# Performance work log

Hardware: AMD Instinct MI355X
Metric: run time of the kernel (lower is better)

## Reference

```python
import jax, jax.numpy as jnp
import numpy as np

COST_CLASS, COST_BBOX, COST_GIOU = 2.0, 5.0, 2.0
ALPHA, GAMMA = 0.25, 2.0
EPS = 1e-8
N_CANDIDATE = 10


def box_cxcywh_to_xyxy(b):
    cx, cy, w, h = b[..., 0], b[..., 1], b[..., 2], b[..., 3]
    return jnp.stack([cx - 0.5 * w, cy - 0.5 * h, cx + 0.5 * w, cy + 0.5 * h], axis=-1)


def pairwise_iou_giou(b1, b2):
    # b1: [N,4] xyxy, b2: [M,4] xyxy -> iou [N,M], giou [N,M]
    area1 = (b1[:, 2] - b1[:, 0]) * (b1[:, 3] - b1[:, 1])
    area2 = (b2[:, 2] - b2[:, 0]) * (b2[:, 3] - b2[:, 1])
    lt = jnp.maximum(b1[:, None, :2], b2[None, :, :2])
    rb = jnp.minimum(b1[:, None, 2:], b2[None, :, 2:])
    wh = jnp.clip(rb - lt, 0.0)
    inter = wh[..., 0] * wh[..., 1]
    union = area1[:, None] + area2[None, :] - inter
    iou = inter / (union + EPS)
    # smallest enclosing box
    lt_c = jnp.minimum(b1[:, None, :2], b2[None, :, :2])
    rb_c = jnp.maximum(b1[:, None, 2:], b2[None, :, 2:])
    wh_c = jnp.clip(rb_c - lt_c, 0.0)
    area_c = wh_c[..., 0] * wh_c[..., 1]
    giou = iou - (area_c - union) / (area_c + EPS)
    return iou, giou


def _match_one(logits, boxes, labels, tboxes):
    # logits [Q,C], boxes [Q,4] cxcywh, labels [G] int, tboxes [G,4] cxcywh
    Q = logits.shape[0]
    G = labels.shape[0]
    prob = jax.nn.sigmoid(logits)                 # [Q,C]  (use_focal_loss path)
    p = prob[:, labels]                           # [Q,G] gather at GT classes
    neg_cost = (1.0 - ALPHA) * p ** GAMMA * (-jnp.log1p(-p + EPS))
    pos_cost = ALPHA * (1.0 - p) ** GAMMA * (-jnp.log(p + EPS))
    cost_class = pos_cost - neg_cost              # [Q,G]
    cost_bbox = jnp.sum(jnp.abs(boxes[:, None, :] - tboxes[None, :, :]), axis=-1)  # L1 cdist [Q,G]
    iou, giou = pairwise_iou_giou(box_cxcywh_to_xyxy(boxes), box_cxcywh_to_xyxy(tboxes))
    C = COST_BBOX * cost_bbox + COST_CLASS * cost_class + COST_GIOU * (-giou)      # [Q,G]

    # --- SimOTA matching (simota_matching), vectorized over GT ---
    cost = C.T                                    # [G,Q]
    ious = iou.T                                  # [G,Q]
    n_cand = min(N_CANDIDATE, Q)
    topk_ious, _ = jax.lax.top_k(ious, n_cand)    # [G,n_cand]
    dynamic_ks = jnp.clip(jnp.sum(topk_ious, axis=1).astype(jnp.int32), 1)  # [G]
    # rank of each anchor per GT under ascending cost
    ranks = jnp.argsort(jnp.argsort(cost, axis=1), axis=1)                  # [G,Q]
    matching = (ranks < dynamic_ks[:, None]).astype(cost.dtype)             # [G,Q]
    # resolve anchors matched to multiple GTs: keep argmin-cost GT
    anchor_matching_gt = matching.sum(axis=0)     # [Q]
    cost_argmin = jnp.argmin(cost, axis=0)        # [Q]
    onehot_min = (jnp.arange(G)[:, None] == cost_argmin[None, :]).astype(cost.dtype)
    matching = jnp.where(anchor_matching_gt[None, :] > 1, onehot_min, matching)
    return jnp.stack([cost, matching], axis=0)    # [2,G,Q]


def reference(pred_logits, pred_boxes, tgt_labels, tgt_boxes):
    # per-image cost blocks + SimOTA matching matrices: [bs, 2, G, Q]
    return jax.vmap(_match_one)(pred_logits, pred_boxes, tgt_labels, tgt_boxes)


def setup_inputs() -> dict:
    key = jax.random.key(0)
    k1, k2, k3, k4 = jax.random.split(key, 4)
    bs, Q, C, G = 16, 4000, 80, 128
    pred_logits = jax.random.normal(k1, (bs, Q, C), dtype=jnp.float32)
    pred_boxes = jax.random.uniform(k2, (bs, Q, 4), dtype=jnp.float32, minval=0.05, maxval=0.95)
    tgt_labels = jax.random.randint(k3, (bs, G), 0, C)
    tgt_boxes = jax.random.uniform(k4, (bs, G, 4), dtype=jnp.float32, minval=0.05, maxval=0.95)
    return {"pred_logits": pred_logits, "pred_boxes": pred_boxes,
            "tgt_labels": tgt_labels, "tgt_boxes": tgt_boxes}
```

## Files before the change

### kernel.cpp

```cpp
#include <hip/hip_runtime.h>
#include <cmath>
#include <cfloat>
#include <climits>


static constexpr int BS = 16;
static constexpr int Qn = 4000;
static constexpr int Cn = 80;
static constexpr int Gn = 128;
static constexpr float kEPS = 1e-8f;


static constexpr size_t kThrvOff = 0;
static constexpr size_t kThriOff = 8 * 1024;
static constexpr size_t kFOff    = 16 * 1024;
static constexpr size_t kFBytes  = (size_t)BS * Cn * Qn * sizeof(float);

__device__ __forceinline__ float focal_cost(float l) {
    const float p = 1.0f / (1.0f + expf(-l));
    const float neg = (0.75f * (p * p)) * (-log1pf(-p + kEPS));
    const float pos = (0.25f * ((1.0f - p) * (1.0f - p))) * (-logf(p + kEPS));
    return pos - neg;
}

__global__ __launch_bounds__(256) void kP_focal(
    const float* __restrict__ logits,
    float* __restrict__ F)
{
    const int b  = blockIdx.y;
    const int q0 = blockIdx.x * 32;
    const int t  = threadIdx.x;

    __shared__ float s_f[32 * 81];

    const float* src = logits + ((size_t)b * Qn + q0) * Cn;
#pragma unroll
    for (int i = 0; i < 10; ++i) {
        const int idx = t + i * 256;
        const int ql = idx / 80, c = idx % 80;
        s_f[ql * 81 + c] = focal_cost(src[idx]);
    }
    __syncthreads();

    float* dst = F + (size_t)b * Cn * Qn;
#pragma unroll
    for (int i = 0; i < 10; ++i) {
        const int j = t + i * 256;
        const int c = j >> 5, ql = j & 31;
        dst[(size_t)c * Qn + q0 + ql] = s_f[ql * 81 + c];
    }
}

__device__ __forceinline__ unsigned long long pack_ci(float c, int q) {
    const unsigned int u = __float_as_uint(c + 0.0f);
    const unsigned int s = (u & 0x80000000u) ? ~u : (u | 0x80000000u);
    return ((unsigned long long)s << 32) | (unsigned int)q;
}

__device__ __forceinline__ unsigned long long shfl_xor_u64(unsigned long long v, int m) {
    const int lo = __shfl_xor((int)(unsigned int)v, m, 64);
    const int hi = __shfl_xor((int)(unsigned int)(v >> 32), m, 64);
    return ((unsigned long long)(unsigned int)hi << 32) | (unsigned int)lo;
}

__device__ __forceinline__ unsigned long long bitonic64_asc_u64(unsigned long long v, int lane) {
#pragma unroll
    for (int k = 2; k <= 64; k <<= 1) {
#pragma unroll
        for (int j = 32; j >= 1; j >>= 1) {
            if (j < k) {
                const unsigned long long o = shfl_xor_u64(v, j);
                const bool up = ((lane & k) == 0);
                const bool keepmin = (((lane & j) == 0) == up);
                const bool omin = (o < v);
                v = (keepmin == omin) ? o : v;
            }
        }
    }
    return v;
}

__device__ __forceinline__ float bitonic64_asc_f32(float v, int lane) {
#pragma unroll
    for (int k = 2; k <= 64; k <<= 1) {
#pragma unroll
        for (int j = 32; j >= 1; j >>= 1) {
            if (j < k) {
                const float o = __shfl_xor(v, j, 64);
                const bool up = ((lane & k) == 0);
                const bool keepmin = (((lane & j) == 0) == up);
                const bool omin = (o < v);
                v = (keepmin == omin) ? o : v;
            }
        }
    }
    return v;
}

__device__ __forceinline__ void ins10_vi(float (&cv)[10], int (&ci)[10],
                                         float v, int q) {
    bool le[10];
#pragma unroll
    for (int j = 0; j < 10; ++j) le[j] = (cv[j] <= v);
#pragma unroll
    for (int j = 9; j >= 1; --j) {
        const float nv = le[j] ? cv[j] : (le[j - 1] ? v : cv[j - 1]);
        const int   ni = le[j] ? ci[j] : (le[j - 1] ? q : ci[j - 1]);
        cv[j] = nv; ci[j] = ni;
    }
    if (!le[0]) { cv[0] = v; ci[0] = q; }
}

__device__ __forceinline__ void ins10_desc(float (&iv)[10], float v) {
    bool ge[10];
#pragma unroll
    for (int j = 0; j < 10; ++j) ge[j] = (iv[j] >= v);
#pragma unroll
    for (int j = 9; j >= 1; --j)
        iv[j] = ge[j] ? iv[j] : (ge[j - 1] ? v : iv[j - 1]);
    if (!ge[0]) iv[0] = v;
}

template <bool USE_F>
__global__ __launch_bounds__(512, 8) void kF(
    const float* __restrict__ boxes,
    const int*   __restrict__ labels,
    const float* __restrict__ tboxes,
    const float* __restrict__ logits,
    const float* __restrict__ F,
    float* __restrict__ out,
    float* __restrict__ thrv,
    int*   __restrict__ thri)
{
    const int lane = threadIdx.x & 63;
    const int w8   = threadIdx.x >> 6;
    const int sub  = w8 & 3;
    const int r    = blockIdx.x;
    const int b    = r >> 7;
    const int g    = r & (Gn - 1);

    const float* tb = tboxes + (size_t)r * 4;
    const float tcx = tb[0], tcy = tb[1], tw = tb[2], th = tb[3];
    const float tx0 = tcx - 0.5f * tw, ty0 = tcy - 0.5f * th;
    const float tx1 = tcx + 0.5f * tw, ty1 = tcy + 0.5f * th;
    const float tarea = (tx1 - tx0) * (ty1 - ty0);

    const float4* brow = reinterpret_cast<const float4*>(boxes) + (size_t)b * Qn;

    __shared__ float              s_st[8][1024];
    __shared__ unsigned long long s_ccb[4][64];
    __shared__ float              s_icb[4][64];
    __shared__ int                s_cnt[8];
    __shared__ unsigned long long s_ce[4][12];
    __shared__ float              s_if[4][12];

    if (lane == 0) s_cnt[w8] = 0;

    if (w8 < 4) {
        const int lab = labels[r];
        const float* Frow = USE_F ? (F + ((size_t)b * Cn + lab) * Qn) : nullptr;
        const float* lcol = USE_F ? nullptr : (logits + (size_t)b * Qn * Cn + lab);
        float* crow = out + (size_t)(b * 2) * Gn * Qn + (size_t)g * Qn;

        float m0 = INFINITY, m1 = INFINITY;

#pragma unroll
        for (int it = 0; it < 4; ++it) {
            const int q0 = it * 1024 + sub * 256 + (lane << 2);
            if ((it < 3) || (q0 < Qn)) {
                float cls4[4];
                if (USE_F) {
                    const float4 f4 = *reinterpret_cast<const float4*>(Frow + q0);
                    cls4[0] = f4.x; cls4[1] = f4.y; cls4[2] = f4.z; cls4[3] = f4.w;
                } else {
#pragma unroll
                    for (int e = 0; e < 4; ++e)
                        cls4[e] = focal_cost(lcol[(size_t)(q0 + e) * Cn]);
                }
                float c4[4];
#pragma unroll
                for (int e = 0; e < 4; ++e) {
                    const float cls = cls4[e];
                    const float4 bb = brow[q0 + e];
                    const float cx = bb.x, cy = bb.y, w = bb.z, h = bb.w;
                    const float x0 = cx - 0.5f * w, y0 = cy - 0.5f * h;
                    const float x1 = cx + 0.5f * w, y1 = cy + 0.5f * h;
                    const float area1 = (x1 - x0) * (y1 - y0);
                    const float l1 = ((fabsf(cx - tcx) + fabsf(cy - tcy))
                                      + fabsf(w - tw)) + fabsf(h - th);
                    const float ltx = fmaxf(x0, tx0), lty = fmaxf(y0, ty0);
                    const float rbx = fminf(x1, tx1), rby = fminf(y1, ty1);
                    const float iw = fmaxf(rbx - ltx, 0.0f), ih = fmaxf(rby - lty, 0.0f);
                    const float inter = iw * ih;
                    const float uni = (area1 + tarea) - inter;
                    const float iou = inter / (uni + kEPS);
                    const float cltx = fminf(x0, tx0), clty = fminf(y0, ty0);
                    const float crbx = fmaxf(x1, tx1), crby = fmaxf(y1, ty1);
                    const float cw = fmaxf(crbx - cltx, 0.0f), ch = fmaxf(crby - clty, 0.0f);
                    const float areac = cw * ch;
                    const float giou = iou - (areac - uni) / (areac + kEPS);

                    const float cost = (5.0f * l1 + 2.0f * cls) + 2.0f * (-giou);
                    c4[e] = cost;
                    const bool le0 = (m0 <= cost), le1 = (m1 <= cost);
                    m1 = le1 ? m1 : (le0 ? cost : m0);
                    m0 = le0 ? m0 : cost;
                }
                float4 cv4; cv4.x = c4[0]; cv4.y = c4[1]; cv4.z = c4[2]; cv4.w = c4[3];
                *reinterpret_cast<float4*>(crow + q0) = cv4;
                *reinterpret_cast<float4*>(&s_st[w8][it * 256 + (lane << 2)]) = cv4;
            }
        }

        float T = 0.0f;
#pragma unroll
        for (int t = 0; t < 10; ++t) {
            float m = m0;
#pragma unroll
            for (int d = 1; d <= 32; d <<= 1)
                m = fminf(m, __shfl_xor(m, d, 64));
            T = m;
            const bool own0 = (m0 == m);
            const unsigned long long bal = __ballot(own0);
            if (own0 && lane == __ffsll((long long)bal) - 1) { m0 = m1; m1 = INFINITY; }
        }

#pragma unroll
        for (int it = 0; it < 4; ++it) {
            const int q0 = it * 1024 + sub * 256 + (lane << 2);
            if ((it < 3) || (q0 < Qn)) {
                const float4 c4 = *reinterpret_cast<const float4*>(
                    &s_st[w8][it * 256 + (lane << 2)]);
#pragma unroll
                for (int e = 0; e < 4; ++e) {
                    const float c = (e == 0) ? c4.x : (e == 1) ? c4.y
                                  : (e == 2) ? c4.z : c4.w;
                    if (c <= T) {
                        const int slot = atomicAdd(&s_cnt[w8], 1);
                        if (slot < 64) s_ccb[sub][slot] = pack_ci(c, q0 + e);
                    }
                }
            }
        }

        const int cnt = s_cnt[w8];
        if (cnt <= 64) {
            unsigned long long v = (lane < cnt) ? s_ccb[sub][lane] : ~0ull;
            v = bitonic64_asc_u64(v, lane);
            if (lane < 12) s_ce[sub][lane] = (lane < 10) ? v : ~0ull;
        } else {
            float cv[10]; int ci[10];
#pragma unroll
            for (int j = 0; j < 10; ++j) { cv[j] = INFINITY; ci[j] = INT_MAX; }
#pragma unroll
            for (int it = 0; it < 4; ++it) {
                const int q0 = it * 1024 + sub * 256 + (lane << 2);
                if ((it < 3) || (q0 < Qn)) {
                    const float4 c4 = *reinterpret_cast<const float4*>(
                        &s_st[w8][it * 256 + (lane << 2)]);
                    ins10_vi(cv, ci, c4.x, q0);
                    ins10_vi(cv, ci, c4.y, q0 + 1);
                    ins10_vi(cv, ci, c4.z, q0 + 2);
                    ins10_vi(cv, ci, c4.w, q0 + 3);
                }
            }
#pragma unroll
            for (int t = 0; t < 10; ++t) {
                float m = cv[0];
#pragma unroll
                for (int d = 1; d <= 32; d <<= 1)
                    m = fminf(m, __shfl_xor(m, d, 64));
                int cq = (cv[0] == m) ? ci[0] : INT_MAX;
#pragma unroll
                for (int d = 1; d <= 32; d <<= 1)
                    cq = min(cq, __shfl_xor(cq, d, 64));
                if (lane == 0) s_ce[sub][t] = pack_ci(m, cq);
                const bool own = (cv[0] == m) && (ci[0] == cq);
                if (own) {
#pragma unroll
                    for (int j = 0; j < 9; ++j) { cv[j] = cv[j + 1]; ci[j] = ci[j + 1]; }
                    cv[9] = INFINITY; ci[9] = INT_MAX;
                }
            }
            if (lane < 2) s_ce[sub][10 + lane] = ~0ull;
        }
    } else {
        float M0 = -INFINITY, M1 = -INFINITY;

#pragma unroll
        for (int it = 0; it < 4; ++it) {
            const int q0 = it * 1024 + sub * 256 + (lane << 2);
            if ((it < 3) || (q0 < Qn)) {
                float io4[4];
#pragma unroll
                for (int e = 0; e < 4; ++e) {
                    const float4 bb = brow[q0 + e];
                    const float x0 = bb.x - 0.5f * bb.z, y0 = bb.y - 0.5f * bb.w;
                    const float x1 = bb.x + 0.5f * bb.z, y1 = bb.y + 0.5f * bb.w;
                    const float area1 = (x1 - x0) * (y1 - y0);
                    const float ltx = fmaxf(x0, tx0), lty = fmaxf(y0, ty0);
                    const float rbx = fminf(x1, tx1), rby = fminf(y1, ty1);
                    const float iw = fmaxf(rbx - ltx, 0.0f), ih = fmaxf(rby - lty, 0.0f);
                    const float inter = iw * ih;
                    const float uni = (area1 + tarea) - inter;
                    const float iou = inter / (uni + kEPS);
                    io4[e] = iou;
                    const bool ge0 = (M0 >= iou), ge1 = (M1 >= iou);
                    M1 = ge1 ? M1 : (ge0 ? iou : M0);
                    M0 = ge0 ? M0 : iou;
                }
                float4 iv4; iv4.x = io4[0]; iv4.y = io4[1]; iv4.z = io4[2]; iv4.w = io4[3];
                *reinterpret_cast<float4*>(&s_st[w8][it * 256 + (lane << 2)]) = iv4;
            }
        }

        float T = 0.0f;
#pragma unroll
        for (int t = 0; t < 10; ++t) {
            float m = M0;
#pragma unroll
            for (int d = 1; d <= 32; d <<= 1)
                m = fmaxf(m, __shfl_xor(m, d, 64));
            T = m;
            const bool own0 = (M0 == m);
            const unsigned long long bal = __ballot(own0);
            if (own0 && lane == __ffsll((long long)bal) - 1) { M0 = M1; M1 = -INFINITY; }
        }

#pragma unroll
        for (int it = 0; it < 4; ++it) {
            const int q0 = it * 1024 + sub * 256 + (lane << 2);
            if ((it < 3) || (q0 < Qn)) {
                const float4 c4 = *reinterpret_cast<const float4*>(
                    &s_st[w8][it * 256 + (lane << 2)]);
#pragma unroll
                for (int e = 0; e < 4; ++e) {
                    const float c = (e == 0) ? c4.x : (e == 1) ? c4.y
                                  : (e == 2) ? c4.z : c4.w;
                    if (c >= T) {
                        const int slot = atomicAdd(&s_cnt[w8], 1);
                        if (slot < 64) s_icb[sub][slot] = c;
                    }
                }
            }
        }

        const int cnt = s_cnt[w8];
        if (cnt <= 64) {
            float v = (lane < cnt) ? s_icb[sub][lane] : -INFINITY;
            v = bitonic64_asc_f32(v, lane);
            if (lane >= 54) s_if[sub][63 - lane] = v;
            if (lane < 2) s_if[sub][10 + lane] = -INFINITY;
        } else {
            float iv[10];
#pragma unroll
            for (int j = 0; j < 10; ++j) iv[j] = -INFINITY;
#pragma unroll
            for (int it = 0; it < 4; ++it) {
                const int q0 = it * 1024 + sub * 256 + (lane << 2);
                if ((it < 3) || (q0 < Qn)) {
                    const float4 c4 = *reinterpret_cast<const float4*>(
                        &s_st[w8][it * 256 + (lane << 2)]);
                    ins10_desc(iv, c4.x);
                    ins10_desc(iv, c4.y);
                    ins10_desc(iv, c4.z);
                    ins10_desc(iv, c4.w);
                }
            }
#pragma unroll
            for (int t = 0; t < 10; ++t) {
                float m = iv[0];
#pragma unroll
                for (int d = 1; d <= 32; d <<= 1)
                    m = fmaxf(m, __shfl_xor(m, d, 64));
                if (lane == 0) s_if[sub][t] = m;
                const bool own0 = (iv[0] == m);
                const unsigned long long bal = __ballot(own0);
                if (own0 && lane == __ffsll((long long)bal) - 1) {
#pragma unroll
                    for (int j = 0; j < 9; ++j) iv[j] = iv[j + 1];
                    iv[9] = -INFINITY;
                }
            }
            if (lane < 2) s_if[sub][10 + lane] = -INFINITY;
        }
    }

    __syncthreads();

    if (threadIdx.x == 0) {
        int p0 = 0, p1 = 0, p2 = 0, p3 = 0;
        float s = 0.0f;
#pragma unroll
        for (int t = 0; t < 10; ++t) {
            const float a0 = s_if[0][p0], a1 = s_if[1][p1];
            const float a2 = s_if[2][p2], a3 = s_if[3][p3];
            const float mx = fmaxf(fmaxf(a0, a1), fmaxf(a2, a3));
            if (a0 == mx) ++p0;
            else if (a1 == mx) ++p1;
            else if (a2 == mx) ++p2;
            else ++p3;
            s += mx;
        }
        int k = (int)s;
        if (k < 1) k = 1;
        if (k > 10) k = 10;

        p0 = 0; p1 = 0; p2 = 0; p3 = 0;
        unsigned long long key = 0;
#pragma unroll
        for (int t = 0; t < 10; ++t) {
            const unsigned long long a0 = s_ce[0][p0], a1 = s_ce[1][p1];
            const unsigned long long a2 = s_ce[2][p2], a3 = s_ce[3][p3];
            unsigned long long mn = a0;
            if (a1 < mn) mn = a1;
            if (a2 < mn) mn = a2;
            if (a3 < mn) mn = a3;
            if (a0 == mn) ++p0;
            else if (a1 == mn) ++p1;
            else if (a2 == mn) ++p2;
            else ++p3;
            if (t == k - 1) key = mn;
        }
        const unsigned int su = (unsigned int)(key >> 32);
        thrv[r] = __uint_as_float((su & 0x80000000u) ? (su ^ 0x80000000u) : ~su);
        thri[r] = (int)(unsigned int)key;
    }
}

__global__ __launch_bounds__(512) void kC5(
    const float* __restrict__ outc,
    const float* __restrict__ thrv,
    const int*   __restrict__ thri,
    float* __restrict__ out)
{
    const int b    = blockIdx.y;
    const int lane = threadIdx.x & 63;
    const int gh   = threadIdx.x >> 6;
    const int quad = blockIdx.x * 64 + lane;
    const int q0   = quad * 4;

    __shared__ float              s_tv[Gn];
    __shared__ int                s_ti[Gn];
    __shared__ unsigned long long s_mask[8][64];
    __shared__ float              s_mv0[8][64], s_mv1[8][64];
    __shared__ float              s_mv2[8][64], s_mv3[8][64];
    __shared__ unsigned           s_mg[8][64];

    if (threadIdx.x < Gn) {
        s_tv[threadIdx.x] = thrv[b * Gn + threadIdx.x];
        s_ti[threadIdx.x] = thri[b * Gn + threadIdx.x];
    }
    __syncthreads();

    const bool act = (quad < Qn / 4);
    const int gbase = gh * 16;
    unsigned long long mask = 0;
    float mv0 = INFINITY, mv1 = INFINITY, mv2 = INFINITY, mv3 = INFINITY;
    int mg0 = 0, mg1 = 0, mg2 = 0, mg3 = 0;

    if (act) {
        const float* crow = outc + (size_t)(b * 2) * Gn * Qn + q0;
#pragma unroll
        for (int j = 0; j < 16; ++j) {
            const int g = gbase + j;
            const float4 c = *reinterpret_cast<const float4*>(crow + (size_t)g * Qn);
            const float tvg = s_tv[g];
            const int   tig = s_ti[g];
            const bool t0 = (c.x < tvg) || (c.x == tvg && q0     <= tig);
            const bool t1 = (c.y < tvg) || (c.y == tvg && q0 + 1 <= tig);
            const bool t2 = (c.z < tvg) || (c.z == tvg && q0 + 2 <= tig);
            const bool t3 = (c.w < tvg) || (c.w == tvg && q0 + 3 <= tig);
            mask |= ((unsigned long long)t0 << j)
                  | ((unsigned long long)t1 << (16 + j))
                  | ((unsigned long long)t2 << (32 + j))
                  | ((unsigned long long)t3 << (48 + j));
            if (c.x < mv0) { mv0 = c.x; mg0 = g; }
            if (c.y < mv1) { mv1 = c.y; mg1 = g; }
            if (c.z < mv2) { mv2 = c.z; mg2 = g; }
            if (c.w < mv3) { mv3 = c.w; mg3 = g; }
        }
    }
    s_mask[gh][lane] = mask;
    s_mv0[gh][lane] = mv0; s_mv1[gh][lane] = mv1;
    s_mv2[gh][lane] = mv2; s_mv3[gh][lane] = mv3;
    s_mg[gh][lane] = (unsigned)mg0 | ((unsigned)mg1 << 8)
                   | ((unsigned)mg2 << 16) | ((unsigned)mg3 << 24);
    __syncthreads();

    int c0 = 0, c1 = 0, c2 = 0, c3 = 0;
#pragma unroll
    for (int h = 0; h < 8; ++h) {
        const unsigned long long m = s_mask[h][lane];
        c0 += __popcll(m & 0xFFFFull);
        c1 += __popcll((m >> 16) & 0xFFFFull);
        c2 += __popcll((m >> 32) & 0xFFFFull);
        c3 += __popcll((m >> 48) & 0xFFFFull);
    }
    float b0 = s_mv0[0][lane], b1 = s_mv1[0][lane];
    float b2 = s_mv2[0][lane], b3 = s_mv3[0][lane];
    unsigned pk = s_mg[0][lane];
    int g0b = pk & 0xFF, g1b = (pk >> 8) & 0xFF;
    int g2b = (pk >> 16) & 0xFF, g3b = (pk >> 24) & 0xFF;
#pragma unroll
    for (int h = 1; h < 8; ++h) {
        const unsigned pkh = s_mg[h][lane];
        const float v0 = s_mv0[h][lane];
        if (v0 < b0) { b0 = v0; g0b = pkh & 0xFF; }
        const float v1 = s_mv1[h][lane];
        if (v1 < b1) { b1 = v1; g1b = (pkh >> 8) & 0xFF; }
        const float v2 = s_mv2[h][lane];
        if (v2 < b2) { b2 = v2; g2b = (pkh >> 16) & 0xFF; }
        const float v3 = s_mv3[h][lane];
        if (v3 < b3) { b3 = v3; g3b = (pkh >> 24) & 0xFF; }
    }
    const bool f0 = (c0 > 1), f1 = (c1 > 1), f2 = (c2 > 1), f3 = (c3 > 1);

    if (act) {
        float* mrow = out + (size_t)(b * 2 + 1) * Gn * Qn + q0;
#pragma unroll
        for (int j = 0; j < 16; ++j) {
            const int g = gbase + j;
            float4 o;
            o.x = (f0 ? (g == g0b) : ((mask >> j) & 1ull))        ? 1.0f : 0.0f;
            o.y = (f1 ? (g == g1b) : ((mask >> (16 + j)) & 1ull)) ? 1.0f : 0.0f;
            o.z = (f2 ? (g == g2b) : ((mask >> (32 + j)) & 1ull)) ? 1.0f : 0.0f;
            o.w = (f3 ? (g == g3b) : ((mask >> (48 + j)) & 1ull)) ? 1.0f : 0.0f;
            *reinterpret_cast<float4*>(mrow + (size_t)g * Qn) = o;
        }
    }
}

extern "C" void kernel_launch(void* const* d_in, const int* in_sizes, int n_in,
                              void* d_out, int out_size, void* d_ws, size_t ws_size,
                              hipStream_t stream) {
    (void)in_sizes; (void)n_in; (void)out_size;
    const float* logits = (const float*)d_in[0];
    const float* boxes  = (const float*)d_in[1];
    const int*   labels = (const int*)d_in[2];
    const float* tboxes = (const float*)d_in[3];
    float* out = (float*)d_out;

    float* thrv = (float*)((char*)d_ws + kThrvOff);
    int*   thri = (int*)  ((char*)d_ws + kThriOff);
    float* F    = (float*)((char*)d_ws + kFOff);

    const bool use_f = (ws_size >= kFOff + kFBytes);

    dim3 gF(BS * Gn);
    if (use_f) {
        dim3 gP(Qn / 32, BS);
        kP_focal<<<gP, 256, 0, stream>>>(logits, F);
        kF<true><<<gF, 512, 0, stream>>>(boxes, labels, tboxes, logits, F,
                                         out, thrv, thri);
    } else {
        kF<false><<<gF, 512, 0, stream>>>(boxes, labels, tboxes, logits, nullptr,
                                          out, thrv, thri);
    }

    dim3 gC((Qn / 4 + 63) / 64, BS);
    kC5<<<gC, 512, 0, stream>>>(out, thrv, thri, out);
}
```

Baseline: 76.81 us.

## Replace dense matching pass with sparse claim scatter and conflict resolution

The dense kC5 pass, which rebuilds the matching plane by comparing every (g,q) cost against per-GT thresholds, is replaced by a sparse path. kF now records up to k matched anchor indices per GT. A scatter kernel then atomically counts claims per anchor and records the claiming GT. A final kernel writes ones for singly-claimed anchors and does a column argmin only for contested ones, after a separate zero-fill of the matching plane. This avoids re-reading the full cost plane, at the price of three extra launches, a full zero-write and atomics. The packed claim word assumes fewer than 256 claims per anchor. Tie-handling may also differ from the threshold-based path.

```diff
diff --git a/kernel.cpp b/kernel.cpp
--- a/kernel.cpp
+++ b/kernel.cpp
@@ -11,10 +11,14 @@
 static constexpr float kEPS = 1e-8f;
 
 
-static constexpr size_t kThrvOff = 0;
-static constexpr size_t kThriOff = 8 * 1024;
-static constexpr size_t kFOff    = 16 * 1024;
-static constexpr size_t kFBytes  = (size_t)BS * Cn * Qn * sizeof(float);
+static constexpr size_t kKOff     = 0;
+static constexpr size_t kThrvOff  = 8 * 1024;
+static constexpr size_t kThriOff  = 16 * 1024;
+static constexpr size_t kMatOff   = 24 * 1024;
+static constexpr size_t kClaimOff = 112 * 1024;
+static constexpr size_t kFOff     = 384 * 1024;
+static constexpr size_t kFfbOff   = 24 * 1024;
+static constexpr size_t kFBytes   = (size_t)BS * Cn * Qn * sizeof(float);
 
 __device__ __forceinline__ float focal_cost(float l) {
     const float p = 1.0f / (1.0f + expf(-l));
@@ -130,7 +134,9 @@
     const float* __restrict__ F,
     float* __restrict__ out,
     float* __restrict__ thrv,
-    int*   __restrict__ thri)
+    int*   __restrict__ thri,
+    int*   __restrict__ kkp,
+    int*   __restrict__ matched)
 {
     const int lane = threadIdx.x & 63;
     const int w8   = threadIdx.x >> 6;
@@ -421,11 +427,73 @@
             else if (a2 == mn) ++p2;
             else ++p3;
             if (t == k - 1) key = mn;
+            if (matched != nullptr && t < k)
+                matched[(size_t)r * 10 + t] = (int)(unsigned int)mn;
         }
         const unsigned int su = (unsigned int)(key >> 32);
         thrv[r] = __uint_as_float((su & 0x80000000u) ? (su ^ 0x80000000u) : ~su);
         thri[r] = (int)(unsigned int)key;
-    }
+        if (kkp != nullptr) kkp[r] = k;
+    }
+}
+
+__global__ __launch_bounds__(256) void kZ_zero(
+    float* __restrict__ out,
+    unsigned* __restrict__ claims)
+{
+    const int b = blockIdx.y;
+    const int i = blockIdx.x * 256 + threadIdx.x;
+    float4 z; z.x = 0.0f; z.y = 0.0f; z.z = 0.0f; z.w = 0.0f;
+    float* plane = out + (size_t)(b * 2 + 1) * Gn * Qn;
+    *reinterpret_cast<float4*>(plane + (size_t)i * 4) = z;
+    if (i < Qn / 4) {
+        uint4 u; u.x = 0; u.y = 0; u.z = 0; u.w = 0;
+        *reinterpret_cast<uint4*>(claims + (size_t)b * Qn + i * 4) = u;
+    }
+}
+
+__global__ __launch_bounds__(256) void kS_scatter(
+    const int* __restrict__ kkp,
+    const int* __restrict__ matched,
+    unsigned* __restrict__ claims)
+{
+    const int id = blockIdx.x * 256 + threadIdx.x;
+    const int r = id / 10, j = id % 10;
+    if (j < kkp[r]) {
+        const int q = matched[(size_t)r * 10 + j];
+        const int b = r >> 7;
+        const int g = r & (Gn - 1);
+        atomicAdd(&claims[(size_t)b * Qn + q], 1u | ((unsigned)g << 8));
+    }
+}
+
+__global__ __launch_bounds__(256) void kM_mat(
+    const float* __restrict__ outc,
+    const unsigned* __restrict__ claims,
+    float* __restrict__ out)
+{
+    const int b = blockIdx.y;
+    const int q = blockIdx.x * 256 + threadIdx.x;
+    if (q >= Qn) return;
+
+    const unsigned v = claims[(size_t)b * Qn + q];
+    const unsigned cnt = v & 0xFFu;
+    if (cnt == 0u) return;
+
+    float* plane = out + (size_t)(b * 2 + 1) * Gn * Qn;
+    if (cnt == 1u) {
+        const int g = (int)(v >> 8);
+        plane[(size_t)g * Qn + q] = 1.0f;
+        return;
+    }
+    const float* crow = outc + (size_t)(b * 2) * Gn * Qn + q;
+    float mv = INFINITY;
+    int mg = 0;
+    for (int g = 0; g < Gn; ++g) {
+        const float c = crow[(size_t)g * Qn];
+        if (c < mv) { mv = c; mg = g; }
+    }
+    plane[(size_t)mg * Qn + q] = 1.0f;
 }
 
 __global__ __launch_bounds__(512) void kC5(
@@ -541,23 +609,45 @@
     const float* tboxes = (const float*)d_in[3];
     float* out = (float*)d_out;
 
-    float* thrv = (float*)((char*)d_ws + kThrvOff);
-    int*   thri = (int*)  ((char*)d_ws + kThriOff);
-    float* F    = (float*)((char*)d_ws + kFOff);
-
-    const bool use_f = (ws_size >= kFOff + kFBytes);
+    int*      kkp     = (int*)     ((char*)d_ws + kKOff);
+    float*    thrv    = (float*)   ((char*)d_ws + kThrvOff);
+    int*      thri    = (int*)     ((char*)d_ws + kThriOff);
+    int*      matched = (int*)     ((char*)d_ws + kMatOff);
+    unsigned* claims  = (unsigned*)((char*)d_ws + kClaimOff);
+
+    const bool full = (ws_size >= kFOff + kFBytes);
+    const bool fb   = (ws_size >= kFfbOff + kFBytes);
 
     dim3 gF(BS * Gn);
-    if (use_f) {
+    if (full) {
+        float* F = (float*)((char*)d_ws + kFOff);
+
+        dim3 gZ(Gn * Qn / 4 / 256, BS);
+        kZ_zero<<<gZ, 256, 0, stream>>>(out, claims);
+
+        dim3 gP(Qn / 32, BS);
+        kP_focal<<<gP, 256, 0, stream>>>(logits, F);
+
+        kF<true><<<gF, 512, 0, stream>>>(boxes, labels, tboxes, logits, F,
+                                         out, thrv, thri, kkp, matched);
+
+        dim3 gS((BS * Gn * 10 + 255) / 256);
+        kS_scatter<<<gS, 256, 0, stream>>>(kkp, matched, claims);
+
+        dim3 gM((Qn + 255) / 256, BS);
+        kM_mat<<<gM, 256, 0, stream>>>(out, claims, out);
+    } else if (fb) {
+        float* F = (float*)((char*)d_ws + kFfbOff);
         dim3 gP(Qn / 32, BS);
         kP_focal<<<gP, 256, 0, stream>>>(logits, F);
         kF<true><<<gF, 512, 0, stream>>>(boxes, labels, tboxes, logits, F,
-                                         out, thrv, thri);
+                                         out, thrv, thri, nullptr, nullptr);
+        dim3 gC((Qn / 4 + 63) / 64, BS);
+        kC5<<<gC, 512, 0, stream>>>(out, thrv, thri, out);
     } else {
         kF<false><<<gF, 512, 0, stream>>>(boxes, labels, tboxes, logits, nullptr,
-                                          out, thrv, thri);
-    }
-
-    dim3 gC((Qn / 4 + 63) / 64, BS);
-    kC5<<<gC, 512, 0, stream>>>(out, thrv, thri, out);
-}
+                                          out, thrv, thri, nullptr, nullptr);
+        dim3 gC((Qn / 4 + 63) / 64, BS);
+        kC5<<<gC, 512, 0, stream>>>(out, thrv, thri, out);
+    }
+}
```

Measured after the change: 83.15 us. 8.3% more time.
